# Optimization experiments

Measured on AMD Instinct MI355X. Metric: run time of the kernel, lower is better.

Reference implementation:

```python
import jax, jax.numpy as jnp
from jax import lax
import numpy as np

MB, N, QST, EPS = 512, 25, 11, 1e-5

def _coords():
    i = np.arange(25)
    # faithful to python3 true division: (i/5 - 2)/2.0, (i%5 - 2)/2.0
    c = np.stack([(i / 5 - 2) / 2.0, (i % 5 - 2) / 2.0], axis=-1).astype(np.float32)
    return jnp.asarray(c)  # [25, 2]

def _conv_bn(x, w, b, g, beta):
    # Conv2d(k=3, stride=2, pad=1) -> ReLU -> BatchNorm (training-mode batch stats)
    y = lax.conv_general_dilated(x, w, (2, 2), [(1, 1), (1, 1)],
                                 dimension_numbers=('NCHW', 'OIHW', 'NCHW'))
    y = jax.nn.relu(y + b[None, :, None, None])
    mean = y.mean(axis=(0, 2, 3), keepdims=True)
    var = y.var(axis=(0, 2, 3), keepdims=True)
    return (y - mean) * jax.lax.rsqrt(var + EPS) * g[None, :, None, None] + beta[None, :, None, None]

def setup_inputs() -> dict:
    key = jax.random.key(0)
    ks = jax.random.split(key, 20)
    w = lambda k, s: jax.random.normal(k, s, jnp.float32) * 0.05
    inp = {
        'img': jax.random.normal(ks[0], (MB, 3, 75, 75), jnp.float32),
        'qst': jax.random.normal(ks[1], (MB, QST), jnp.float32),
        'c1w': w(ks[2], (24, 3, 3, 3)),  'c1b': jnp.zeros((24,)), 'bn1g': jnp.ones((24,)), 'bn1b': jnp.zeros((24,)),
        'c2w': w(ks[3], (24, 24, 3, 3)), 'c2b': jnp.zeros((24,)), 'bn2g': jnp.ones((24,)), 'bn2b': jnp.zeros((24,)),
        'c3w': w(ks[4], (24, 24, 3, 3)), 'c3b': jnp.zeros((24,)), 'bn3g': jnp.ones((24,)), 'bn3b': jnp.zeros((24,)),
        'c4w': w(ks[5], (24, 24, 3, 3)), 'c4b': jnp.zeros((24,)), 'bn4g': jnp.ones((24,)), 'bn4b': jnp.zeros((24,)),
        'gw1': w(ks[6], (256, 63)),  'gb1': jnp.zeros((256,)),
        'gw2': w(ks[7], (256, 256)), 'gb2': jnp.zeros((256,)),
        'gw3': w(ks[8], (256, 256)), 'gb3': jnp.zeros((256,)),
        'gw4': w(ks[9], (256, 256)), 'gb4': jnp.zeros((256,)),
        'fw1': w(ks[10], (256, 256)), 'fb1': jnp.zeros((256,)),
        'fw2': w(ks[11], (256, 256)), 'fb2': jnp.zeros((256,)),
        'fw3': w(ks[12], (10, 256)),  'fb3': jnp.zeros((10,)),
    }
    return inp

def reference(img, qst, c1w, c1b, bn1g, bn1b, c2w, c2b, bn2g, bn2b,
              c3w, c3b, bn3g, bn3b, c4w, c4b, bn4g, bn4b,
              gw1, gb1, gw2, gb2, gw3, gb3, gw4, gb4,
              fw1, fb1, fw2, fb2, fw3, fb3):
    x = _conv_bn(img, c1w, c1b, bn1g, bn1b)
    x = _conv_bn(x, c2w, c2b, bn2g, bn2b)
    x = _conv_bn(x, c3w, c3b, bn3g, bn3b)
    x = _conv_bn(x, c4w, c4b, bn4g, bn4b)  # [mb, 24, 5, 5]
    mb, C = x.shape[0], x.shape[1]
    n = x.shape[2] * x.shape[3]
    xf = x.reshape(mb, C, n).transpose(0, 2, 1)              # [mb, N, 24]
    coord = jnp.broadcast_to(_coords()[None], (mb, n, 2))
    xf = jnp.concatenate([xf, coord], axis=-1)               # [mb, N, 26]
    qrep = jnp.broadcast_to(qst[:, None, :], (mb, n, QST))
    xj = jnp.concatenate([xf, qrep], axis=-1)                # [mb, N, 37]
    # pair[b,a,c] = [xf[b,c], xf[b,a], qst[b]]  (x_i varies over axis 2, x_j over axis 1)
    pair = jnp.concatenate([
        jnp.broadcast_to(xf[:, None, :, :], (mb, n, n, xf.shape[-1])),
        jnp.broadcast_to(xj[:, :, None, :], (mb, n, n, xj.shape[-1])),
    ], axis=-1)                                              # [mb, N, N, 63]
    h = pair.reshape(mb * n * n, -1)
    for w, b in ((gw1, gb1), (gw2, gb2), (gw3, gb3), (gw4, gb4)):
        h = jax.nn.relu(h @ w.T + b)
    xg = h.reshape(mb, n * n, 256).sum(axis=1)               # sum pooling over pairs
    y = jax.nn.relu(xg @ fw1.T + fb1)
    y = jax.nn.relu(y @ fw2.T + fb2)   # dropout treated as identity (eval mode)
    y = y @ fw3.T + fb3
    return jax.nn.log_softmax(y, axis=-1)
```

## Files before the change

kernel.cpp:

```cpp
#include <hip/hip_runtime.h>

typedef __bf16 bf16_t;
typedef __bf16 bf16x8 __attribute__((ext_vector_type(8)));
typedef __bf16 bf16x4 __attribute__((ext_vector_type(4)));
typedef float f32x16 __attribute__((ext_vector_type(16)));

#define MB 512
#define GROWS 128
#define GT_PER_B 5

__global__ __launch_bounds__(256, 2) void conv1_bn(const float* __restrict__ img,
                                                   const float* __restrict__ wT,
                                                   const float* __restrict__ bias,
                                                   float* __restrict__ out,
                                                   float* __restrict__ statsOut)
{
    __shared__ float in_s[3 * 39 * 77];
    __shared__ float red[48];
    int bid = blockIdx.x;
    int n = bid >> 1, tile = bid & 1;
    int oh0 = tile * 19;
    int tid = threadIdx.x;

    for (int idx = tid; idx < 3 * 39 * 77; idx += 256) {
        int ci = idx / (39 * 77);
        int rem = idx - ci * (39 * 77);
        int r = rem / 77, c = rem - r * 77;
        int ih = 2 * oh0 - 1 + r, iw = c - 1;
        float v = 0.f;
        if ((unsigned)ih < 75u && (unsigned)iw < 75u)
            v = img[((n * 3 + ci) * 75 + ih) * 75 + iw];
        in_s[idx] = v;
    }
    __syncthreads();

    int cg = tid >> 6, lane = tid & 63, co0 = cg * 6;
    int off[12];
    bool pv[12];
#pragma unroll
    for (int j = 0; j < 12; ++j) {
        int p = lane + j * 64;
        pv[j] = p < 722;
        int pc = pv[j] ? p : 0;
        int r0 = pc / 38, c0 = pc - r0 * 38;
        off[j] = (r0 * 2) * 77 + c0 * 2;
    }
    float acc[6][12];
#pragma unroll
    for (int c = 0; c < 6; ++c)
#pragma unroll
        for (int j = 0; j < 12; ++j) acc[c][j] = 0.f;

#pragma unroll 1
    for (int ci = 0; ci < 3; ++ci) {
        const float* ip = in_s + ci * (39 * 77);
        const float* wp = wT + ci * 9 * 24 + co0;
#pragma unroll
        for (int kh = 0; kh < 3; ++kh) {
#pragma unroll
            for (int kw = 0; kw < 3; ++kw) {
                float iv[12];
#pragma unroll
                for (int j = 0; j < 12; ++j) iv[j] = ip[off[j] + kh * 77 + kw];
                const float* wr = wp + (kh * 3 + kw) * 24;
                float2 w01 = *(const float2*)(wr);
                float2 w23 = *(const float2*)(wr + 2);
                float2 w45 = *(const float2*)(wr + 4);
#pragma unroll
                for (int j = 0; j < 12; ++j) {
                    acc[0][j] = fmaf(iv[j], w01.x, acc[0][j]);
                    acc[1][j] = fmaf(iv[j], w01.y, acc[1][j]);
                    acc[2][j] = fmaf(iv[j], w23.x, acc[2][j]);
                    acc[3][j] = fmaf(iv[j], w23.y, acc[3][j]);
                    acc[4][j] = fmaf(iv[j], w45.x, acc[4][j]);
                    acc[5][j] = fmaf(iv[j], w45.y, acc[5][j]);
                }
            }
        }
    }

    float sst[6], sq[6];
#pragma unroll
    for (int c = 0; c < 6; ++c) { sst[c] = 0.f; sq[c] = 0.f; }
#pragma unroll
    for (int c = 0; c < 6; ++c) {
        float bv = bias[co0 + c];
#pragma unroll
        for (int j = 0; j < 12; ++j) {
            if (pv[j]) {
                int p = lane + j * 64;
                int r = p / 38, q = p - r * 38;
                float v = fmaxf(acc[c][j] + bv, 0.f);
                out[((n * 24 + co0 + c) * 38 + oh0 + r) * 38 + q] = v;
                sst[c] += v; sq[c] += v * v;
            }
        }
    }
#pragma unroll
    for (int o = 1; o < 64; o <<= 1) {
#pragma unroll
        for (int c = 0; c < 6; ++c) {
            sst[c] += __shfl_xor(sst[c], o);
            sq[c]  += __shfl_xor(sq[c], o);
        }
    }
    if (lane == 0) {
#pragma unroll
        for (int c = 0; c < 6; ++c) {
            red[(co0 + c) * 2]     = sst[c];
            red[(co0 + c) * 2 + 1] = sq[c];
        }
    }
    __syncthreads();
    if (tid < 48) atomicAdd(&statsOut[tid], red[tid]);
}

template <int HIN, int WIN, int HOUT, int WOUT, int OHT, int NP>
__global__ __launch_bounds__(256, 2) void conv24_bn(const float* __restrict__ in,
                                                    const float* __restrict__ wT,
                                                    const float* __restrict__ bias,
                                                    const float* __restrict__ statsIn,
                                                    const float* __restrict__ gIn,
                                                    const float* __restrict__ bIn, float invcntIn,
                                                    float* __restrict__ out,
                                                    float* __restrict__ statsOut, int tilesPerImg)
{
    constexpr int IR = 2 * OHT + 1;
    constexpr int ICW = 2 * WOUT + 1;
    __shared__ float in_s[24 * IR * ICW];
    __shared__ float aff[48];
    __shared__ float red[48];

    int bid = blockIdx.x;
    int n = bid / tilesPerImg, tile = bid - n * tilesPerImg;
    int oh0 = tile * OHT;
    int tid = threadIdx.x;

    if (tid < 24) {
        float mean = statsIn[tid * 2] * invcntIn;
        float var  = statsIn[tid * 2 + 1] * invcntIn - mean * mean;
        float s    = gIn[tid] * rsqrtf(var + 1e-5f);
        aff[tid * 2] = s;
        aff[tid * 2 + 1] = bIn[tid] - mean * s;
    }
    __syncthreads();
    for (int idx = tid; idx < 24 * IR * ICW; idx += 256) {
        int ci = idx / (IR * ICW);
        int rem = idx - ci * (IR * ICW);
        int r = rem / ICW, c = rem - r * ICW;
        int ih = 2 * oh0 - 1 + r, iw = c - 1;
        float v = 0.f;
        if ((unsigned)ih < (unsigned)HIN && (unsigned)iw < (unsigned)WIN)
            v = aff[ci * 2] * in[((n * 24 + ci) * HIN + ih) * WIN + iw] + aff[ci * 2 + 1];
        in_s[idx] = v;
    }
    __syncthreads();

    int cg = tid >> 6, lane = tid & 63, co0 = cg * 6;
    int nvr = HOUT - oh0; if (nvr > OHT) nvr = OHT;
    int nposv = nvr * WOUT;
    int off[NP];
    bool pv[NP];
#pragma unroll
    for (int j = 0; j < NP; ++j) {
        int p = lane + j * 64;
        pv[j] = p < nposv;
        int pc = pv[j] ? p : 0;
        int r0 = pc / WOUT, c0 = pc - r0 * WOUT;
        off[j] = (r0 * 2) * ICW + c0 * 2;
    }
    float acc[6][NP];
#pragma unroll
    for (int c = 0; c < 6; ++c)
#pragma unroll
        for (int j = 0; j < NP; ++j) acc[c][j] = 0.f;

#pragma unroll 1
    for (int ci = 0; ci < 24; ++ci) {
        const float* ip = in_s + ci * (IR * ICW);
        const float* wp = wT + ci * 9 * 24 + co0;
#pragma unroll
        for (int kh = 0; kh < 3; ++kh) {
#pragma unroll
            for (int kw = 0; kw < 3; ++kw) {
                float iv[NP];
#pragma unroll
                for (int j = 0; j < NP; ++j) iv[j] = ip[off[j] + kh * ICW + kw];
                const float* wr = wp + (kh * 3 + kw) * 24;
                float2 w01 = *(const float2*)(wr);
                float2 w23 = *(const float2*)(wr + 2);
                float2 w45 = *(const float2*)(wr + 4);
#pragma unroll
                for (int j = 0; j < NP; ++j) {
                    acc[0][j] = fmaf(iv[j], w01.x, acc[0][j]);
                    acc[1][j] = fmaf(iv[j], w01.y, acc[1][j]);
                    acc[2][j] = fmaf(iv[j], w23.x, acc[2][j]);
                    acc[3][j] = fmaf(iv[j], w23.y, acc[3][j]);
                    acc[4][j] = fmaf(iv[j], w45.x, acc[4][j]);
                    acc[5][j] = fmaf(iv[j], w45.y, acc[5][j]);
                }
            }
        }
    }

    float sst[6], sq[6];
#pragma unroll
    for (int c = 0; c < 6; ++c) { sst[c] = 0.f; sq[c] = 0.f; }
#pragma unroll
    for (int c = 0; c < 6; ++c) {
        float bv = bias[co0 + c];
#pragma unroll
        for (int j = 0; j < NP; ++j) {
            if (pv[j]) {
                int p = lane + j * 64;
                int r = p / WOUT, q = p - r * WOUT;
                float v = fmaxf(acc[c][j] + bv, 0.f);
                out[((n * 24 + co0 + c) * HOUT + oh0 + r) * WOUT + q] = v;
                sst[c] += v; sq[c] += v * v;
            }
        }
    }
#pragma unroll
    for (int o = 1; o < 64; o <<= 1) {
#pragma unroll
        for (int c = 0; c < 6; ++c) {
            sst[c] += __shfl_xor(sst[c], o);
            sq[c]  += __shfl_xor(sq[c], o);
        }
    }
    if (lane == 0) {
#pragma unroll
        for (int c = 0; c < 6; ++c) {
            red[(co0 + c) * 2]     = sst[c];
            red[(co0 + c) * 2 + 1] = sq[c];
        }
    }
    __syncthreads();
    if (tid < 48) atomicAdd(&statsOut[tid], red[tid]);
}

__global__ void build_features(const float* __restrict__ y4, const float* __restrict__ stats4,
                               const float* __restrict__ g4, const float* __restrict__ b4,
                               const float* __restrict__ qst,
                               bf16_t* __restrict__ xf26, bf16_t* __restrict__ qstb)
{
    int idx = blockIdx.x * 256 + threadIdx.x;
    if (idx < MB * 11) qstb[idx] = (bf16_t)qst[idx];
    if (idx >= MB * 25) return;
    int b = idx / 25, p = idx % 25;
    const float invcnt = 1.f / (MB * 25);
#pragma unroll
    for (int ch = 0; ch < 24; ++ch) {
        float mean = stats4[ch * 2] * invcnt;
        float var  = stats4[ch * 2 + 1] * invcnt - mean * mean;
        float s    = g4[ch] * rsqrtf(var + 1e-5f);
        float v    = s * y4[(b * 24 + ch) * 25 + p] + (b4[ch] - mean * s);
        xf26[idx * 26 + ch] = (bf16_t)v;
    }
    xf26[idx * 26 + 24] = (bf16_t)((p / 5.0f - 2.0f) * 0.5f);
    xf26[idx * 26 + 25] = (bf16_t)(((float)(p % 5) - 2.0f) * 0.5f);
}

__device__ __forceinline__ void frag256(int idx, const float* __restrict__ gw, bf16_t* __restrict__ Wf)
{
    int j = idx & 7, lane = (idx >> 3) & 63, ks = (idx >> 9) & 15, nt = idx >> 13;
    int n = nt * 32 + (lane & 31), k = ks * 16 + (lane >> 5) * 8 + j;
    Wf[idx] = (bf16_t)gw[n * 256 + k];
}

__global__ void prep_weights(const float* __restrict__ gw1, const float* __restrict__ gw2,
                             const float* __restrict__ gw3, const float* __restrict__ gw4,
                             const float* __restrict__ fw1, const float* __restrict__ fw2,
                             const float* __restrict__ c1w, const float* __restrict__ c2w,
                             const float* __restrict__ c3w, const float* __restrict__ c4w,
                             bf16_t* __restrict__ W1f, bf16_t* __restrict__ W2f,
                             bf16_t* __restrict__ W3f, bf16_t* __restrict__ W4f,
                             float* __restrict__ fw1T, float* __restrict__ fw2T,
                             float* __restrict__ wT1, float* __restrict__ wT2,
                             float* __restrict__ wT3, float* __restrict__ wT4)
{
    int idx = blockIdx.x * 256 + threadIdx.x;
    if (idx < 16384) {
        int j = idx & 7, lane = (idx >> 3) & 63, ks = (idx >> 9) & 3, nt = idx >> 11;
        int n = nt * 32 + (lane & 31), k = ks * 16 + (lane >> 5) * 8 + j;
        W1f[idx] = (k < 63) ? (bf16_t)gw1[n * 63 + k] : (bf16_t)0.0f;
        return;
    }
    idx -= 16384;
    if (idx < 65536) { frag256(idx, gw2, W2f); return; }
    idx -= 65536;
    if (idx < 65536) { frag256(idx, gw3, W3f); return; }
    idx -= 65536;
    if (idx < 65536) { frag256(idx, gw4, W4f); return; }
    idx -= 65536;
    if (idx < 65536) { int k = idx >> 8, nn = idx & 255; fw1T[idx] = fw1[nn * 256 + k]; return; }
    idx -= 65536;
    if (idx < 65536) { int k = idx >> 8, nn = idx & 255; fw2T[idx] = fw2[nn * 256 + k]; return; }
    idx -= 65536;
    if (idx < 648)   { int k = idx / 24, co = idx - k * 24; wT1[idx] = c1w[co * 27 + k]; return; }
    idx -= 648;
    if (idx < 5184)  { int k = idx / 24, co = idx - k * 24; wT2[idx] = c2w[co * 216 + k]; return; }
    idx -= 5184;
    if (idx < 5184)  { int k = idx / 24, co = idx - k * 24; wT3[idx] = c3w[co * 216 + k]; return; }
    idx -= 5184;
    if (idx < 5184)  { int k = idx / 24, co = idx - k * 24; wT4[idx] = c4w[co * 216 + k]; return; }
}


template <int NKS>
__device__ __forceinline__ void g_layer(const bf16_t* hs, const bf16_t* __restrict__ Wf,
                                        int wid, int lane, f32x16 acc[4][2])
{
    int m31 = lane & 31, half = lane >> 5;
#pragma unroll
    for (int mt = 0; mt < 4; ++mt)
#pragma unroll
        for (int nt = 0; nt < 2; ++nt) acc[mt][nt] = (f32x16)(0.f);
#pragma unroll
    for (int ks = 0; ks < NKS; ++ks) {
        int kc = ks * 2 + half;
        bf16x8 hf[4];
#pragma unroll
        for (int mt = 0; mt < 4; ++mt) {
            int m = mt * 32 + m31;
            hf[mt] = *(const bf16x8*)(hs + m * 256 + ((kc ^ m31) << 3));
        }
        bf16x8 wf[2];
#pragma unroll
        for (int nt = 0; nt < 2; ++nt)
            wf[nt] = *(const bf16x8*)(Wf + (size_t)(((wid * 2 + nt) * NKS + ks) * 64 + lane) * 8);
#pragma unroll
        for (int nt = 0; nt < 2; ++nt)
#pragma unroll
            for (int mt = 0; mt < 4; ++mt)
                acc[mt][nt] = __builtin_amdgcn_mfma_f32_32x32x16_bf16(wf[nt], hf[mt], acc[mt][nt], 0, 0, 0);
    }
}

__device__ __forceinline__ void g_store(bf16_t* hs, const float* __restrict__ bias,
                                        int wid, int lane, f32x16 acc[4][2])
{
    int m31 = lane & 31, half = lane >> 5;
#pragma unroll
    for (int mt = 0; mt < 4; ++mt) {
        int m = mt * 32 + m31;
#pragma unroll
        for (int nt = 0; nt < 2; ++nt) {
            int nbase = (wid * 2 + nt) * 32;
#pragma unroll
            for (int g = 0; g < 4; ++g) {
                int n0 = nbase + g * 8 + half * 4;
                float4 bv = *(const float4*)(bias + n0);
                bf16x4 v;
                v[0] = (bf16_t)fmaxf(acc[mt][nt][g * 4 + 0] + bv.x, 0.f);
                v[1] = (bf16_t)fmaxf(acc[mt][nt][g * 4 + 1] + bv.y, 0.f);
                v[2] = (bf16_t)fmaxf(acc[mt][nt][g * 4 + 2] + bv.z, 0.f);
                v[3] = (bf16_t)fmaxf(acc[mt][nt][g * 4 + 3] + bv.w, 0.f);
                int chunk = n0 >> 3;
                *(bf16x4*)(hs + m * 256 + ((chunk ^ m31) << 3) + (half << 2)) = v;
            }
        }
    }
}

__global__ void __launch_bounds__(256, 2)
g_mlp(const bf16_t* __restrict__ xf26, const bf16_t* __restrict__ qstb,
      const bf16_t* __restrict__ W1f, const bf16_t* __restrict__ W2f,
      const bf16_t* __restrict__ W3f, const bf16_t* __restrict__ W4f,
      const float* __restrict__ b1, const float* __restrict__ b2,
      const float* __restrict__ b3, const float* __restrict__ b4,
      float* __restrict__ xg)
{
    __shared__ __align__(16) bf16_t hs[GROWS * 256];
    int b    = blockIdx.x / GT_PER_B;
    int tile = blockIdx.x % GT_PER_B;
    int tid  = threadIdx.x;

    for (int i = tid; i < GROWS * 8; i += 256) {
        int m = i >> 3, c = i & 7;
        int p = tile * GROWS + m;
        bf16x8 v;
        if (p < 625) {
            int a = p / 25, cp = p - a * 25;
            const bf16_t* f1 = xf26 + (b * 25 + cp) * 26;
            const bf16_t* f2 = xf26 + (b * 25 + a) * 26;
            const bf16_t* f3 = qstb + b * 11;
#pragma unroll
            for (int j = 0; j < 8; ++j) {
                int col = c * 8 + j;
                bf16_t u = (bf16_t)0.0f;
                if (col < 26) u = f1[col];
                else if (col < 52) u = f2[col - 26];
                else if (col < 63) u = f3[col - 52];
                v[j] = u;
            }
        } else {
#pragma unroll
            for (int j = 0; j < 8; ++j) v[j] = (bf16_t)0.0f;
        }
        *(bf16x8*)(hs + m * 256 + ((c ^ (m & 31)) << 3)) = v;
    }
    __syncthreads();

    int wid = tid >> 6, lane = tid & 63;
    int m31 = lane & 31, half = lane >> 5;
    f32x16 acc[4][2];

    g_layer<4>(hs, W1f, wid, lane, acc);
    __syncthreads(); g_store(hs, b1, wid, lane, acc); __syncthreads();
    g_layer<16>(hs, W2f, wid, lane, acc);
    __syncthreads(); g_store(hs, b2, wid, lane, acc); __syncthreads();
    g_layer<16>(hs, W3f, wid, lane, acc);
    __syncthreads(); g_store(hs, b3, wid, lane, acc); __syncthreads();
    g_layer<16>(hs, W4f, wid, lane, acc);

#pragma unroll
    for (int nt = 0; nt < 2; ++nt) {
        int nbase = (wid * 2 + nt) * 32;
        float bf[16];
#pragma unroll
        for (int r = 0; r < 16; ++r)
            bf[r] = b4[nbase + (r & 3) + 8 * (r >> 2) + 4 * half];
        f32x16 t = (f32x16)(0.f);
#pragma unroll
        for (int mt = 0; mt < 4; ++mt) {
            int p = tile * GROWS + mt * 32 + m31;
            if (p < 625) {
#pragma unroll
                for (int r = 0; r < 16; ++r)
                    t[r] += fmaxf(acc[mt][nt][r] + bf[r], 0.f);
            }
        }
#pragma unroll
        for (int off = 1; off < 32; off <<= 1) {
#pragma unroll
            for (int r = 0; r < 16; ++r) t[r] += __shfl_xor(t[r], off);
        }
        if (m31 == 0) {
#pragma unroll
            for (int r = 0; r < 16; ++r) {
                int nn = nbase + (r & 3) + 8 * (r >> 2) + 4 * half;
                atomicAdd(&xg[b * 256 + nn], t[r]);
            }
        }
    }
}

__global__ void f_mlp(const float* __restrict__ xg, const float* __restrict__ fw1T, const float* __restrict__ fb1,
                      const float* __restrict__ fw2T, const float* __restrict__ fb2,
                      const float* __restrict__ fw3, const float* __restrict__ fb3,
                      float* __restrict__ out)
{
    __shared__ float xa[256], xb[256], lg[10];
    int b = blockIdx.x, t = threadIdx.x;
    xa[t] = xg[b * 256 + t];
    __syncthreads();
    float a = fb1[t];
    for (int k = 0; k < 256; ++k) a += fw1T[k * 256 + t] * xa[k];
    xb[t] = fmaxf(a, 0.f);
    __syncthreads();
    a = fb2[t];
    for (int k = 0; k < 256; ++k) a += fw2T[k * 256 + t] * xb[k];
    xa[t] = fmaxf(a, 0.f);
    __syncthreads();
    if (t < 10) {
        float s = fb3[t];
        for (int k = 0; k < 256; ++k) s += fw3[t * 256 + k] * xa[k];
        lg[t] = s;
    }
    __syncthreads();
    if (t == 0) {
        float m = lg[0];
        for (int i = 1; i < 10; ++i) m = fmaxf(m, lg[i]);
        float s = 0.f;
        for (int i = 0; i < 10; ++i) s += expf(lg[i] - m);
        float ls = m + logf(s);
        for (int i = 0; i < 10; ++i) out[b * 10 + i] = lg[i] - ls;
    }
}

extern "C" void kernel_launch(void* const* d_in, const int* in_sizes, int n_in,
                              void* d_out, int out_size, void* d_ws, size_t ws_size,
                              hipStream_t stream)
{
    (void)in_sizes; (void)n_in; (void)out_size; (void)ws_size;
    const float* img  = (const float*)d_in[0];
    const float* qst  = (const float*)d_in[1];
    const float* c1w  = (const float*)d_in[2];
    const float* c1b  = (const float*)d_in[3];
    const float* bn1g = (const float*)d_in[4];
    const float* bn1b = (const float*)d_in[5];
    const float* c2w  = (const float*)d_in[6];
    const float* c2b  = (const float*)d_in[7];
    const float* bn2g = (const float*)d_in[8];
    const float* bn2b = (const float*)d_in[9];
    const float* c3w  = (const float*)d_in[10];
    const float* c3b  = (const float*)d_in[11];
    const float* bn3g = (const float*)d_in[12];
    const float* bn3b = (const float*)d_in[13];
    const float* c4w  = (const float*)d_in[14];
    const float* c4b  = (const float*)d_in[15];
    const float* bn4g = (const float*)d_in[16];
    const float* bn4b = (const float*)d_in[17];
    const float* gw1  = (const float*)d_in[18];
    const float* gb1  = (const float*)d_in[19];
    const float* gw2  = (const float*)d_in[20];
    const float* gb2  = (const float*)d_in[21];
    const float* gw3  = (const float*)d_in[22];
    const float* gb3  = (const float*)d_in[23];
    const float* gw4  = (const float*)d_in[24];
    const float* gb4  = (const float*)d_in[25];
    const float* fw1  = (const float*)d_in[26];
    const float* fb1  = (const float*)d_in[27];
    const float* fw2  = (const float*)d_in[28];
    const float* fb2  = (const float*)d_in[29];
    const float* fw3  = (const float*)d_in[30];
    const float* fb3  = (const float*)d_in[31];

    const int Y1 = 512 * 24 * 38 * 38;
    const int Y2 = 512 * 24 * 19 * 19;
    const int Y3 = 512 * 24 * 10 * 10;
    const int Y4 = 512 * 24 * 5 * 5;

    float* fp = (float*)d_ws;
    float* y1    = fp;  fp += Y1;
    float* y2    = fp;  fp += Y2;
    float* y3    = fp;  fp += Y3;
    float* y4    = fp;  fp += Y4;
    float* stats = fp;  fp += 192;
    float* xg    = fp;  fp += 512 * 256;
    float* fw1T  = fp;  fp += 65536;
    float* fw2T  = fp;  fp += 65536;
    float* wT1   = fp;  fp += 648;
    float* wT2   = fp;  fp += 5184;
    float* wT3   = fp;  fp += 5184;
    float* wT4   = fp;  fp += 5184;
    bf16_t* bp   = (bf16_t*)fp;
    bf16_t* xf26 = bp;  bp += 512 * 25 * 26;
    bf16_t* qstb = bp;  bp += 512 * 11;
    bf16_t* W1f  = bp;  bp += 16384;
    bf16_t* W2f  = bp;  bp += 65536;
    bf16_t* W3f  = bp;  bp += 65536;
    bf16_t* W4f  = bp;  bp += 65536;

    hipMemsetAsync(stats, 0, 192 * sizeof(float), stream);
    hipMemsetAsync(xg, 0, 512 * 256 * sizeof(float), stream);

    prep_weights<<<1408, 256, 0, stream>>>(gw1, gw2, gw3, gw4, fw1, fw2, c1w, c2w, c3w, c4w,
                                           W1f, W2f, W3f, W4f, fw1T, fw2T,
                                           wT1, wT2, wT3, wT4);

    conv1_bn<<<1024, 256, 0, stream>>>(img, wT1, c1b, y1, stats + 0);

    conv24_bn<38, 38, 19, 19, 5, 2><<<2048, 256, 0, stream>>>(
        y1, wT2, c2b, stats + 0, bn1g, bn1b, 1.f / (512.f * 1444.f),
        y2, stats + 48, 4);

    conv24_bn<19, 19, 10, 10, 10, 2><<<512, 256, 0, stream>>>(
        y2, wT3, c3b, stats + 48, bn2g, bn2b, 1.f / (512.f * 361.f),
        y3, stats + 96, 1);

    conv24_bn<10, 10, 5, 5, 5, 1><<<512, 256, 0, stream>>>(
        y3, wT4, c4b, stats + 96, bn3g, bn3b, 1.f / (512.f * 100.f),
        y4, stats + 144, 1);

    build_features<<<50, 256, 0, stream>>>(y4, stats + 144, bn4g, bn4b, qst, xf26, qstb);

    g_mlp<<<512 * GT_PER_B, 256, 0, stream>>>(xf26, qstb, W1f, W2f, W3f, W4f,
                                              gb1, gb2, gb3, gb4, xg);

    f_mlp<<<512, 256, 0, stream>>>(xg, fw1T, fb1, fw2T, fb2, fw3, fb3, (float*)d_out);
}
```

Measured before the change: 602.5 us.

## Accumulate BN statistics in double and raise conv launch-bound occupancy

```diff
diff --git a/kernel.cpp b/kernel.cpp
--- a/kernel.cpp
+++ b/kernel.cpp
@@ -9,11 +9,11 @@
 #define GROWS 128
 #define GT_PER_B 5
 
-__global__ __launch_bounds__(256, 2) void conv1_bn(const float* __restrict__ img,
+__global__ __launch_bounds__(256, 4) void conv1_bn(const float* __restrict__ img,
                                                    const float* __restrict__ wT,
                                                    const float* __restrict__ bias,
                                                    float* __restrict__ out,
-                                                   float* __restrict__ statsOut)
+                                                   double* __restrict__ statsOut)
 {
     __shared__ float in_s[3 * 39 * 77];
     __shared__ float red[48];
@@ -112,18 +112,18 @@
         }
     }
     __syncthreads();
-    if (tid < 48) atomicAdd(&statsOut[tid], red[tid]);
-}
-
-template <int HIN, int WIN, int HOUT, int WOUT, int OHT, int NP>
-__global__ __launch_bounds__(256, 2) void conv24_bn(const float* __restrict__ in,
+    if (tid < 48) atomicAdd(&statsOut[tid], (double)red[tid]);
+}
+
+template <int HIN, int WIN, int HOUT, int WOUT, int OHT, int NP, int MINW>
+__global__ __launch_bounds__(256, MINW) void conv24_bn(const float* __restrict__ in,
                                                     const float* __restrict__ wT,
                                                     const float* __restrict__ bias,
-                                                    const float* __restrict__ statsIn,
+                                                    const double* __restrict__ statsIn,
                                                     const float* __restrict__ gIn,
                                                     const float* __restrict__ bIn, float invcntIn,
                                                     float* __restrict__ out,
-                                                    float* __restrict__ statsOut, int tilesPerImg)
+                                                    double* __restrict__ statsOut, int tilesPerImg)
 {
     constexpr int IR = 2 * OHT + 1;
     constexpr int ICW = 2 * WOUT + 1;
@@ -137,9 +137,10 @@
     int tid = threadIdx.x;
 
     if (tid < 24) {
-        float mean = statsIn[tid * 2] * invcntIn;
-        float var  = statsIn[tid * 2 + 1] * invcntIn - mean * mean;
-        float s    = gIn[tid] * rsqrtf(var + 1e-5f);
+        double meand = statsIn[tid * 2] * (double)invcntIn;
+        double vard  = statsIn[tid * 2 + 1] * (double)invcntIn - meand * meand;
+        float mean = (float)meand;
+        float s    = gIn[tid] * rsqrtf((float)vard + 1e-5f);
         aff[tid * 2] = s;
         aff[tid * 2 + 1] = bIn[tid] - mean * s;
     }
@@ -236,10 +237,10 @@
         }
     }
     __syncthreads();
-    if (tid < 48) atomicAdd(&statsOut[tid], red[tid]);
-}
-
-__global__ void build_features(const float* __restrict__ y4, const float* __restrict__ stats4,
+    if (tid < 48) atomicAdd(&statsOut[tid], (double)red[tid]);
+}
+
+__global__ void build_features(const float* __restrict__ y4, const double* __restrict__ stats4,
                                const float* __restrict__ g4, const float* __restrict__ b4,
                                const float* __restrict__ qst,
                                bf16_t* __restrict__ xf26, bf16_t* __restrict__ qstb)
@@ -248,12 +249,13 @@
     if (idx < MB * 11) qstb[idx] = (bf16_t)qst[idx];
     if (idx >= MB * 25) return;
     int b = idx / 25, p = idx % 25;
-    const float invcnt = 1.f / (MB * 25);
+    const double invcnt = 1.0 / (MB * 25);
 #pragma unroll
     for (int ch = 0; ch < 24; ++ch) {
-        float mean = stats4[ch * 2] * invcnt;
-        float var  = stats4[ch * 2 + 1] * invcnt - mean * mean;
-        float s    = g4[ch] * rsqrtf(var + 1e-5f);
+        double meand = stats4[ch * 2] * invcnt;
+        double vard  = stats4[ch * 2 + 1] * invcnt - meand * meand;
+        float mean = (float)meand;
+        float s    = g4[ch] * rsqrtf((float)vard + 1e-5f);
         float v    = s * y4[(b * 24 + ch) * 25 + p] + (b4[ch] - mean * s);
         xf26[idx * 26 + ch] = (bf16_t)v;
     }
@@ -522,12 +524,12 @@
     const int Y3 = 512 * 24 * 10 * 10;
     const int Y4 = 512 * 24 * 5 * 5;
 
-    float* fp = (float*)d_ws;
+    double* stats = (double*)d_ws;
+    float* fp = (float*)(stats + 192);
     float* y1    = fp;  fp += Y1;
     float* y2    = fp;  fp += Y2;
     float* y3    = fp;  fp += Y3;
     float* y4    = fp;  fp += Y4;
-    float* stats = fp;  fp += 192;
     float* xg    = fp;  fp += 512 * 256;
     float* fw1T  = fp;  fp += 65536;
     float* fw2T  = fp;  fp += 65536;
@@ -543,7 +545,7 @@
     bf16_t* W3f  = bp;  bp += 65536;
     bf16_t* W4f  = bp;  bp += 65536;
 
-    hipMemsetAsync(stats, 0, 192 * sizeof(float), stream);
+    hipMemsetAsync(stats, 0, 192 * sizeof(double), stream);
     hipMemsetAsync(xg, 0, 512 * 256 * sizeof(float), stream);
 
     prep_weights<<<1408, 256, 0, stream>>>(gw1, gw2, gw3, gw4, fw1, fw2, c1w, c2w, c3w, c4w,
@@ -552,15 +554,15 @@
 
     conv1_bn<<<1024, 256, 0, stream>>>(img, wT1, c1b, y1, stats + 0);
 
-    conv24_bn<38, 38, 19, 19, 5, 2><<<2048, 256, 0, stream>>>(
+    conv24_bn<38, 38, 19, 19, 5, 2, 3><<<2048, 256, 0, stream>>>(
         y1, wT2, c2b, stats + 0, bn1g, bn1b, 1.f / (512.f * 1444.f),
         y2, stats + 48, 4);
 
-    conv24_bn<19, 19, 10, 10, 10, 2><<<512, 256, 0, stream>>>(
+    conv24_bn<19, 19, 10, 10, 10, 2, 3><<<512, 256, 0, stream>>>(
         y2, wT3, c3b, stats + 48, bn2g, bn2b, 1.f / (512.f * 361.f),
         y3, stats + 96, 1);
 
-    conv24_bn<10, 10, 5, 5, 5, 1><<<512, 256, 0, stream>>>(
+    conv24_bn<10, 10, 5, 5, 5, 1, 6><<<512, 256, 0, stream>>>(
         y3, wT4, c4b, stats + 96, bn3g, bn3b, 1.f / (512.f * 100.f),
         y4, stats + 144, 1);
 
```

Result: slower. 653.8 us (+8.5%).
